# Optimization experiments

Hardware: AMD Instinct MI355X
Metric: run time of the kernel (lower is better)

## Reference

```python
import jax, jax.numpy as jnp
import numpy as np

B, IN_SIZE, OUT_SIZE, N_QUBITS, DEPTH = 4096, 512, 256, 12, 3
C64 = jnp.complex64
BN_EPS = 1e-5


def setup_inputs() -> dict:
    key = jax.random.key(0)
    ks = jax.random.split(key, 6)
    x = jax.random.normal(ks[0], (B, IN_SIZE), jnp.float32)
    enc_w = jax.random.normal(ks[1], (N_QUBITS, IN_SIZE), jnp.float32) / np.sqrt(IN_SIZE)
    enc_b = jnp.zeros((N_QUBITS,), jnp.float32)
    rot_params = jax.random.normal(ks[2], (DEPTH, N_QUBITS, 3), jnp.float32) * 0.1
    ent_params = jax.random.normal(ks[3], (DEPTH, N_QUBITS - 1), jnp.float32) * 0.1
    dec_w = jax.random.normal(ks[4], (OUT_SIZE, N_QUBITS), jnp.float32) / np.sqrt(N_QUBITS)
    dec_b = jnp.zeros((OUT_SIZE,), jnp.float32)
    return {
        'x': x, 'enc_w': enc_w, 'enc_b': enc_b,
        'rot_params': rot_params, 'ent_params': ent_params,
        'dec_w': dec_w, 'dec_b': dec_b,
        'bn1_gamma': jnp.ones((N_QUBITS,), jnp.float32),
        'bn1_beta': jnp.zeros((N_QUBITS,), jnp.float32),
        'bn2_gamma': jnp.ones((OUT_SIZE,), jnp.float32),
        'bn2_beta': jnp.zeros((OUT_SIZE,), jnp.float32),
    }


def _m2(a, b, c, d):
    return jnp.stack([jnp.stack([a, b]), jnp.stack([c, d])]).astype(C64)


def _rx(t):
    c = jnp.cos(t / 2).astype(C64)
    s = jnp.sin(t / 2).astype(C64)
    return _m2(c, -1j * s, -1j * s, c)


def _ry(t):
    c = jnp.cos(t / 2)
    s = jnp.sin(t / 2)
    return _m2(c, -s, s, c)


def _rz(p):
    z = jnp.zeros((), C64)
    return _m2(jnp.exp(-1j * p / 2), z, z, jnp.exp(1j * p / 2))


def _apply_1q(state, U, q):
    # state: [B, 2^n]; apply 2x2 U on qubit q (qubit 0 = most significant axis)
    b = state.shape[0]
    s = state.reshape(b, 2 ** q, 2, -1)
    s = jnp.einsum('ij,bkjl->bkil', U, s)
    return s.reshape(b, -1)


def _apply_cry(state, theta, q):
    # controlled-Ry: control qubit q, target qubit q+1 (adjacent)
    b = state.shape[0]
    R = _ry(theta)
    st = state.reshape(b, 2 ** q, 2, 2, -1)
    s0 = st[:, :, 0]
    s1 = jnp.einsum('ij,bkjl->bkil', R, st[:, :, 1])
    return jnp.stack([s0, s1], axis=2).reshape(b, -1)


def _batchnorm(x, g, b):
    # BatchNorm1d in training mode: biased batch stats
    m = x.mean(0)
    v = x.var(0)
    return g * (x - m) / jnp.sqrt(v + BN_EPS) + b


def _quantum_forward(encoded, rot_params, ent_params):
    # Batched statevector simulation of the per-sample circuit.
    b, n = encoded.shape
    depth = rot_params.shape[0]
    # amplitude encoding: normalize, theta = 2*arcsin(clip(|a|,0,1)), P(pi) if a<0
    norm = jnp.linalg.norm(encoded, axis=1, keepdims=True)
    a = jnp.where(norm > 0, encoded / jnp.maximum(norm, 1e-30), encoded)
    amp = jnp.clip(jnp.abs(a), 0.0, 1.0)              # sin(theta/2)
    cos_h = jnp.sqrt(jnp.maximum(1.0 - amp * amp, 0.0))  # cos(theta/2)
    sgn = jnp.where(a < 0, -1.0, 1.0)                  # P(pi) flips sign of |1> amp
    qvec = jnp.stack([cos_h, sgn * amp], axis=-1).astype(C64)  # [B, n, 2]
    # product state via successive outer products (loop over fixed n qubits)
    state = jnp.ones((b, 1), C64)
    for q in range(n):
        state = (state[:, :, None] * qvec[:, q, None, :]).reshape(b, -1)
    # parameterized circuit
    for l in range(depth):
        for q in range(n):
            U = _rz(rot_params[l, q, 2]) @ _ry(rot_params[l, q, 1]) @ _rx(rot_params[l, q, 0])
            state = _apply_1q(state, U, q)
        for q in range(n - 1):
            state = _apply_cry(state, ent_params[l, q], q)
    # per-qubit P(|1>) measurement probabilities
    idx = jnp.arange(2 ** n)
    bits = ((idx[:, None] >> (n - 1 - jnp.arange(n))) & 1).astype(jnp.float32)  # [2^n, n]
    probs = (jnp.abs(state) ** 2).astype(jnp.float32) @ bits  # [B, n]
    return probs


def reference(x, enc_w, enc_b, rot_params, ent_params, dec_w, dec_b,
              bn1_gamma, bn1_beta, bn2_gamma, bn2_beta):
    encoded = x @ enc_w.T + enc_b
    encoded = jnp.tanh(_batchnorm(encoded, bn1_gamma, bn1_beta))
    probs = _quantum_forward(encoded, rot_params, ent_params)
    out = probs @ dec_w.T + dec_b
    return _batchnorm(out, bn2_gamma, bn2_beta)
```

## Files before the change

### kernel.cpp

```cpp
#include <hip/hip_runtime.h>

#define BATCH   4096
#define IN_SZ   512
#define NQ      12
#define OUT_SZ  256
#define DEPTH   3
#define NST     4096
#define BN_EPS  1e-5f

#define OFF_ENC    0
#define OFF_BN1M   49152
#define OFF_BN1R   49168
#define OFF_GU     49184
#define OFF_GC     49472
#define OFF_GF     49568
#define OFF_PROBS  49792
#define OFF_PMEAN  98944
#define OFF_COV    98960
#define OFF_RSTD   99104

typedef float v2f __attribute__((ext_vector_type(2)));
typedef float v4f __attribute__((ext_vector_type(4)));
#define SW2(a) __builtin_shufflevector(a, a, 1, 0)

__global__ void k_encode(const float* __restrict__ x, const float* __restrict__ w,
                         const float* __restrict__ bvec,
                         const float* __restrict__ rot, const float* __restrict__ ent,
                         float* __restrict__ enc, float* __restrict__ gU, float* __restrict__ gC,
                         float* __restrict__ gF) {
    if (blockIdx.x == 1024) {
        int t = threadIdx.x;
        if (t < DEPTH * NQ) {
            float ax = rot[t * 3 + 0] * 0.5f;
            float ay = rot[t * 3 + 1] * 0.5f;
            float az = rot[t * 3 + 2] * 0.5f;
            float cx = cosf(ax), sx = sinf(ax);
            float cy = cosf(ay), sy = sinf(ay);
            float cz = cosf(az), sz = sinf(az);
            float m00r =  cy * cx, m00i =  sy * sx;
            float m01r = -sy * cx, m01i = -cy * sx;
            float m10r =  sy * cx, m10i = -cy * sx;
            float m11r =  cy * cx, m11i = -sy * sx;
            float* o = gU + t * 8;
            o[0] = cz * m00r + sz * m00i;  o[1] = cz * m00i - sz * m00r;
            o[2] = cz * m01r + sz * m01i;  o[3] = cz * m01i - sz * m01r;
            o[4] = cz * m10r - sz * m10i;  o[5] = cz * m10i + sz * m10r;
            o[6] = cz * m11r - sz * m11i;  o[7] = cz * m11i + sz * m11r;
        }
        if (t >= 64 && t - 64 < DEPTH * (NQ - 1)) {
            int i = t - 64;
            float th = ent[i] * 0.5f;
            gC[i * 2 + 0] = cosf(th);
            gC[i * 2 + 1] = sinf(th);
        }
        if (t >= 128 && t - 128 < DEPTH * 9) {
            int i = t - 128;
            int l = i / 9, k = i % 9;
            int c = k + k / 3;
            int tq = c + 1;
            const float* rr = rot + (l * NQ + tq) * 3;
            float ax = rr[0] * 0.5f, ay = rr[1] * 0.5f, az = rr[2] * 0.5f;
            float cx = cosf(ax), sx = sinf(ax);
            float cy = cosf(ay), sy = sinf(ay);
            float cz = cosf(az), sz = sinf(az);
            float m00r =  cy * cx, m00i =  sy * sx;
            float m01r = -sy * cx, m01i = -cy * sx;
            float m10r =  sy * cx, m10i = -cy * sx;
            float m11r =  cy * cx, m11i = -sy * sx;
            float u0 = cz * m00r + sz * m00i, u1 = cz * m00i - sz * m00r;
            float u2 = cz * m01r + sz * m01i, u3 = cz * m01i - sz * m01r;
            float u4 = cz * m10r - sz * m10i, u5 = cz * m10i + sz * m10r;
            float u6 = cz * m11r - sz * m11i, u7 = cz * m11i + sz * m11r;
            float th = ent[l * (NQ - 1) + c] * 0.5f;
            float c_ = cosf(th), s_ = sinf(th);
            float* o = gF + i * 8;
            o[0] = c_ * u0 - s_ * u4;  o[1] = c_ * u1 - s_ * u5;
            o[2] = c_ * u2 - s_ * u6;  o[3] = c_ * u3 - s_ * u7;
            o[4] = s_ * u0 + c_ * u4;  o[5] = s_ * u1 + c_ * u5;
            o[6] = s_ * u2 + c_ * u6;  o[7] = s_ * u3 + c_ * u7;
        }
        return;
    }
    int t = threadIdx.x;
    int wv = t >> 6, lane = t & 63;
    int row = blockIdx.x * 4 + wv;
    const float4* xr = (const float4*)(x + row * IN_SZ) + lane * 2;
    float4 xa = xr[0], xb = xr[1];
    float acc[NQ];
    #pragma unroll
    for (int q = 0; q < NQ; q++) {
        const float4* wr = (const float4*)(w + q * IN_SZ) + lane * 2;
        float4 wa = wr[0], wb = wr[1];
        float d = xa.x*wa.x + xa.y*wa.y + xa.z*wa.z + xa.w*wa.w
                + xb.x*wb.x + xb.y*wb.y + xb.z*wb.z + xb.w*wb.w;
        #pragma unroll
        for (int o = 32; o > 0; o >>= 1) d += __shfl_down(d, o, 64);
        acc[q] = d;
    }
    if (lane == 0) {
        float* er = enc + row * NQ;
        #pragma unroll
        for (int q = 0; q < NQ; q++) er[q] = acc[q] + bvec[q];
    }
}

__device__ float blockAllSum(float v, float* scr) {
    #pragma unroll
    for (int o = 32; o > 0; o >>= 1) v += __shfl_down(v, o, 64);
    int lane = threadIdx.x & 63, w = threadIdx.x >> 6;
    __syncthreads();
    if (lane == 0) scr[w] = v;
    __syncthreads();
    return scr[0] + scr[1] + scr[2] + scr[3];
}

__global__ void k_bnstats(const float* __restrict__ xm, float* __restrict__ mo,
                          float* __restrict__ ro) {
    __shared__ float scr[32];
    int j = blockIdx.x, t = threadIdx.x;
    float s = 0.f, s2 = 0.f;
    for (int b = t; b < BATCH; b += 1024) {
        float v = xm[b * NQ + j];
        s += v; s2 += v * v;
    }
    #pragma unroll
    for (int o = 32; o > 0; o >>= 1) { s += __shfl_down(s, o, 64); s2 += __shfl_down(s2, o, 64); }
    int lane = t & 63, w = t >> 6;
    if (lane == 0) { scr[w] = s; scr[16 + w] = s2; }
    __syncthreads();
    if (t == 0) {
        float S = 0.f, S2 = 0.f;
        #pragma unroll
        for (int i = 0; i < 16; i++) { S += scr[i]; S2 += scr[16 + i]; }
        float mean = S / (float)BATCH;
        float var  = S2 / (float)BATCH - mean * mean;
        mo[j] = mean;
        ro[j] = 1.f / sqrtf(var + BN_EPS);
    }
}

#define SLA2(j) ((T << 4) | ((((j) ^ ((T >> 1) & 7))) << 1))
#define SLB(m)  (((T & 0xF0) << 4) | ((m) << 4) | ((T & 15) ^ ((m) & 14)))
#define SLC(m)  (((m) << 8) | (T ^ ((((T >> 5) & 7)) << 1)))

#define LDA(j, Ra, Rb) { v4f t_ = *(const v4f*)(xch + SLA2(j));                 \
    Ra = __builtin_shufflevector(t_, t_, 0, 1);                                 \
    Rb = __builtin_shufflevector(t_, t_, 2, 3); }
#define STA(j, Ra, Rb) { v4f t_ = __builtin_shufflevector(Ra, Rb, 0, 1, 2, 3);  \
    *(v4f*)(xch + SLA2(j)) = t_; }

#define LOADA do { LDA(0,s0,s1) LDA(1,s2,s3) LDA(2,s4,s5) LDA(3,s6,s7)          \
    LDA(4,s8,s9) LDA(5,s10,s11) LDA(6,s12,s13) LDA(7,s14,s15) } while (0)
#define STORA do { STA(0,s0,s1) STA(1,s2,s3) STA(2,s4,s5) STA(3,s6,s7)          \
    STA(4,s8,s9) STA(5,s10,s11) STA(6,s12,s13) STA(7,s14,s15) } while (0)

#define LOADW(SL) do {                                                          \
    s0=xch[SL(0)];  s1=xch[SL(1)];  s2=xch[SL(2)];  s3=xch[SL(3)];              \
    s4=xch[SL(4)];  s5=xch[SL(5)];  s6=xch[SL(6)];  s7=xch[SL(7)];              \
    s8=xch[SL(8)];  s9=xch[SL(9)];  s10=xch[SL(10)]; s11=xch[SL(11)];           \
    s12=xch[SL(12)]; s13=xch[SL(13)]; s14=xch[SL(14)]; s15=xch[SL(15)]; } while (0)
#define STORW(SL) do {                                                          \
    xch[SL(0)]=s0;  xch[SL(1)]=s1;  xch[SL(2)]=s2;  xch[SL(3)]=s3;              \
    xch[SL(4)]=s4;  xch[SL(5)]=s5;  xch[SL(6)]=s6;  xch[SL(7)]=s7;              \
    xch[SL(8)]=s8;  xch[SL(9)]=s9;  xch[SL(10)]=s10; xch[SL(11)]=s11;           \
    xch[SL(12)]=s12; xch[SL(13)]=s13; xch[SL(14)]=s14; xch[SL(15)]=s15; } while (0)

#define U_LOADP(uptr) const float* u_ = (uptr);                                  \
    v2f c00r = {u_[0], u_[0]}, c00i = {-u_[1], u_[1]};                           \
    v2f c01r = {u_[2], u_[2]}, c01i = {-u_[3], u_[3]};                           \
    v2f c10r = {u_[4], u_[4]}, c10i = {-u_[5], u_[5]};                           \
    v2f c11r = {u_[6], u_[6]}, c11i = {-u_[7], u_[7]};

#define U_LOADF(uptr) const float* f_ = (uptr);                                  \
    v2f d00r = {f_[0], f_[0]}, d00i = {-f_[1], f_[1]};                           \
    v2f d01r = {f_[2], f_[2]}, d01i = {-f_[3], f_[3]};                           \
    v2f d10r = {f_[4], f_[4]}, d10i = {-f_[5], f_[5]};                           \
    v2f d11r = {f_[6], f_[6]}, d11i = {-f_[7], f_[7]};

#define U_PAIRP(A, B) { v2f a0 = A, a1 = B, a0s = SW2(a0), a1s = SW2(a1);        \
    A = a0*c00r + a0s*c00i + a1*c01r + a1s*c01i;                                 \
    B = a0*c10r + a0s*c10i + a1*c11r + a1s*c11i; }

#define U_PAIRF(A, B) { v2f a0 = A, a1 = B, a0s = SW2(a0), a1s = SW2(a1);        \
    A = a0*d00r + a0s*d00i + a1*d01r + a1s*d01i;                                 \
    B = a0*d10r + a0s*d10i + a1*d11r + a1s*d11i; }

#define APPLY_U_K3(uptr) do { U_LOADP(uptr)                                      \
    U_PAIRP(s0,s8) U_PAIRP(s1,s9) U_PAIRP(s2,s10) U_PAIRP(s3,s11)                \
    U_PAIRP(s4,s12) U_PAIRP(s5,s13) U_PAIRP(s6,s14) U_PAIRP(s7,s15) } while (0)

#define APPLY_UF_K2(uP, uF) do { U_LOADP(uP) U_LOADF(uF)                         \
    U_PAIRP(s0,s4) U_PAIRP(s1,s5) U_PAIRP(s2,s6) U_PAIRP(s3,s7)                  \
    U_PAIRF(s8,s12) U_PAIRF(s9,s13) U_PAIRF(s10,s14) U_PAIRF(s11,s15) } while (0)
#define APPLY_UF_K1(uP, uF) do { U_LOADP(uP) U_LOADF(uF)                         \
    U_PAIRP(s0,s2) U_PAIRP(s1,s3) U_PAIRF(s4,s6) U_PAIRF(s5,s7)                  \
    U_PAIRP(s8,s10) U_PAIRP(s9,s11) U_PAIRF(s12,s14) U_PAIRF(s13,s15) } while (0)
#define APPLY_UF_K0(uP, uF) do { U_LOADP(uP) U_LOADF(uF)                         \
    U_PAIRP(s0,s1) U_PAIRF(s2,s3) U_PAIRP(s4,s5) U_PAIRF(s6,s7)                  \
    U_PAIRP(s8,s9) U_PAIRF(s10,s11) U_PAIRP(s12,s13) U_PAIRF(s14,s15) } while (0)

#define RY_PAIRP(A, B) { v2f a0 = A, a1 = B;                                     \
    A = a0*cc2 - a1*ss2;  B = a0*ss2 + a1*cc2; }

#define RYALL_K3(cc, ss) do { v2f cc2 = {(cc),(cc)}, ss2 = {(ss),(ss)};          \
    RY_PAIRP(s0,s8) RY_PAIRP(s1,s9) RY_PAIRP(s2,s10) RY_PAIRP(s3,s11)            \
    RY_PAIRP(s4,s12) RY_PAIRP(s5,s13) RY_PAIRP(s6,s14) RY_PAIRP(s7,s15) } while (0)

#define INITJC(SR, j) { SR.x = f * (((j)&8)?qs0:qc0) * (((j)&4)?qs1:qc1)         \
    * (((j)&2)?qs2:qc2) * (((j)&1)?qs3:qc3); SR.y = 0.f; }
#define PRJ(S) ((S).x*(S).x + (S).y*(S).y)
#define WREDUCE(v) { v += __shfl_down(v,32,64); v += __shfl_down(v,16,64);       \
    v += __shfl_down(v,8,64); v += __shfl_down(v,4,64);                          \
    v += __shfl_down(v,2,64); v += __shfl_down(v,1,64); }

#define MKQ(i) float qc##i, qs##i; {                                             \
    float h_ = h##i;                                                             \
    float a_ = nz ? h_ * rinv : h_;                                              \
    float amp_ = fminf(fabsf(a_), 1.f);                                          \
    qc##i = sqrtf(fmaxf(1.f - amp_ * amp_, 0.f));                                \
    qs##i = (a_ < 0.f) ? -amp_ : amp_; }

__launch_bounds__(256)
__global__ void k_quantum(const float* __restrict__ enc,
                          const float* __restrict__ bn1m, const float* __restrict__ bn1r,
                          const float* __restrict__ g1, const float* __restrict__ b1,
                          const float* __restrict__ gU, const float* __restrict__ gC,
                          const float* __restrict__ gF,
                          float* __restrict__ probs) {
    __shared__ __align__(16) v2f xch[NST];

    int T = threadIdx.x, b = blockIdx.x;

    const float* er = enc + b * NQ;
    float h0  = tanhf(g1[0]  * (er[0]  - bn1m[0])  * bn1r[0]  + b1[0]);
    float h1  = tanhf(g1[1]  * (er[1]  - bn1m[1])  * bn1r[1]  + b1[1]);
    float h2  = tanhf(g1[2]  * (er[2]  - bn1m[2])  * bn1r[2]  + b1[2]);
    float h3  = tanhf(g1[3]  * (er[3]  - bn1m[3])  * bn1r[3]  + b1[3]);
    float h4  = tanhf(g1[4]  * (er[4]  - bn1m[4])  * bn1r[4]  + b1[4]);
    float h5  = tanhf(g1[5]  * (er[5]  - bn1m[5])  * bn1r[5]  + b1[5]);
    float h6  = tanhf(g1[6]  * (er[6]  - bn1m[6])  * bn1r[6]  + b1[6]);
    float h7  = tanhf(g1[7]  * (er[7]  - bn1m[7])  * bn1r[7]  + b1[7]);
    float h8  = tanhf(g1[8]  * (er[8]  - bn1m[8])  * bn1r[8]  + b1[8]);
    float h9  = tanhf(g1[9]  * (er[9]  - bn1m[9])  * bn1r[9]  + b1[9]);
    float h10 = tanhf(g1[10] * (er[10] - bn1m[10]) * bn1r[10] + b1[10]);
    float h11 = tanhf(g1[11] * (er[11] - bn1m[11]) * bn1r[11] + b1[11]);
    float n2 = h0*h0+h1*h1+h2*h2+h3*h3+h4*h4+h5*h5+h6*h6+h7*h7
             + h8*h8+h9*h9+h10*h10+h11*h11;
    float norm = sqrtf(n2);
    bool  nz   = norm > 0.f;
    float rinv = 1.f / fmaxf(norm, 1e-30f);
    MKQ(0) MKQ(1) MKQ(2) MKQ(3) MKQ(4) MKQ(5) MKQ(6) MKQ(7)
    MKQ(8) MKQ(9) MKQ(10) MKQ(11)

    v2f s0, s1, s2, s3, s4, s5, s6, s7, s8, s9, s10, s11, s12, s13, s14, s15;

    {
        float f = ((T>>7)&1 ? qs4 : qc4) * ((T>>6)&1 ? qs5 : qc5)
                * ((T>>5)&1 ? qs6 : qc6) * ((T>>4)&1 ? qs7 : qc7)
                * ((T>>3)&1 ? qs8 : qc8) * ((T>>2)&1 ? qs9 : qc9)
                * ((T>>1)&1 ? qs10 : qc10) * ((T>>0)&1 ? qs11 : qc11);
        INITJC(s0,0)  INITJC(s1,1)  INITJC(s2,2)  INITJC(s3,3)
        INITJC(s4,4)  INITJC(s5,5)  INITJC(s6,6)  INITJC(s7,7)
        INITJC(s8,8)  INITJC(s9,9)  INITJC(s10,10) INITJC(s11,11)
        INITJC(s12,12) INITJC(s13,13) INITJC(s14,14) INITJC(s15,15)
        APPLY_U_K3(gU + 0 * 8);
        APPLY_UF_K2(gU + 1 * 8, gF + 0 * 8);
        APPLY_UF_K1(gU + 2 * 8, gF + 1 * 8);
        APPLY_UF_K0(gU + 3 * 8, gF + 2 * 8);
        STORW(SLC);
    }
    __syncthreads();

    #pragma unroll 1
    for (int l = 0; l < DEPTH; l++) {
        const float* UL = gU + l * 96;
        const float* CL = gC + l * 22;
        const float* FL = gF + l * 72;
        LOADW(SLB);
        APPLY_U_K3(UL + 4 * 8);
        if (T & 16) RYALL_K3(CL[6], CL[7]);
        APPLY_UF_K2(UL + 5 * 8, FL + 3 * 8);
        APPLY_UF_K1(UL + 6 * 8, FL + 4 * 8);
        APPLY_UF_K0(UL + 7 * 8, FL + 5 * 8);
        STORW(SLB);
        __builtin_amdgcn_wave_barrier();
        LOADA;
        APPLY_U_K3(UL + 8 * 8);
        if (T & 1) RYALL_K3(CL[14], CL[15]);
        APPLY_UF_K2(UL + 9 * 8, FL + 6 * 8);
        APPLY_UF_K1(UL + 10 * 8, FL + 7 * 8);
        APPLY_UF_K0(UL + 11 * 8, FL + 8 * 8);
        if (l < DEPTH - 1) {
            STORA;
            __syncthreads();
            const float* UN = gU + (l + 1) * 96;
            const float* FN = gF + (l + 1) * 72;
            LOADW(SLC);
            APPLY_U_K3(UN + 0 * 8);
            APPLY_UF_K2(UN + 1 * 8, FN + 0 * 8);
            APPLY_UF_K1(UN + 2 * 8, FN + 1 * 8);
            APPLY_UF_K0(UN + 3 * 8, FN + 2 * 8);
            STORW(SLC);
            __syncthreads();
        }
    }

    float p0 = PRJ(s0),  p1 = PRJ(s1),  p2 = PRJ(s2),  p3 = PRJ(s3);
    float p4 = PRJ(s4),  p5 = PRJ(s5),  p6 = PRJ(s6),  p7 = PRJ(s7);
    float p8 = PRJ(s8),  p9 = PRJ(s9),  p10 = PRJ(s10), p11 = PRJ(s11);
    float p12 = PRJ(s12), p13 = PRJ(s13), p14 = PRJ(s14), p15 = PRJ(s15);
    float tot = p0+p1+p2+p3+p4+p5+p6+p7+p8+p9+p10+p11+p12+p13+p14+p15;
    float r8  = p8+p9+p10+p11+p12+p13+p14+p15;
    float r9  = p4+p5+p6+p7+p12+p13+p14+p15;
    float r10 = p2+p3+p6+p7+p10+p11+p14+p15;
    float r11 = p1+p3+p5+p7+p9+p11+p13+p15;
    float r0 = (T & 128) ? tot : 0.f;
    float r1 = (T & 64)  ? tot : 0.f;
    float r2 = (T & 32)  ? tot : 0.f;
    float r3 = (T & 16)  ? tot : 0.f;
    float r4 = (T & 8)   ? tot : 0.f;
    float r5 = (T & 4)   ? tot : 0.f;
    float r6 = (T & 2)   ? tot : 0.f;
    float r7 = (T & 1)   ? tot : 0.f;

    WREDUCE(r0) WREDUCE(r1) WREDUCE(r2) WREDUCE(r3) WREDUCE(r4) WREDUCE(r5)
    WREDUCE(r6) WREDUCE(r7) WREDUCE(r8) WREDUCE(r9) WREDUCE(r10) WREDUCE(r11)

    __syncthreads();
    float* red = (float*)xch;
    int lane = T & 63, w = T >> 6;
    if (lane == 0) {
        float* rr = red + w * NQ;
        rr[0]=r0; rr[1]=r1; rr[2]=r2; rr[3]=r3; rr[4]=r4; rr[5]=r5;
        rr[6]=r6; rr[7]=r7; rr[8]=r8; rr[9]=r9; rr[10]=r10; rr[11]=r11;
    }
    __syncthreads();
    if (T < NQ) probs[b * NQ + T] = red[T] + red[NQ + T] + red[2 * NQ + T] + red[3 * NQ + T];
}

__global__ void k_pcov(const float* __restrict__ probs, float* __restrict__ pmean,
                       float* __restrict__ cov) {
    __shared__ float scr[8];
    int blk = blockIdx.x;
    int q = blk / NQ, q2 = blk % NQ;
    int t = threadIdx.x;
    float sx = 0.f, sy = 0.f, sxy = 0.f;
    for (int b = t; b < BATCH; b += 256) {
        float xv = probs[b * NQ + q];
        float yv = probs[b * NQ + q2];
        sx += xv; sy += yv; sxy += xv * yv;
    }
    float SX  = blockAllSum(sx,  scr);
    float SY  = blockAllSum(sy,  scr);
    float SXY = blockAllSum(sxy, scr);
    if (t == 0) {
        float mx = SX / (float)BATCH, my = SY / (float)BATCH;
        cov[blk] = SXY / (float)BATCH - mx * my;
        if (q == q2) pmean[q] = mx;
    }
}

__global__ void k_rstd(const float* __restrict__ cov, const float* __restrict__ dw,
                       float* __restrict__ rstd) {
    __shared__ float cv[NQ * NQ];
    int t = threadIdx.x;
    if (t < NQ * NQ) cv[t] = cov[t];
    __syncthreads();
    float w[NQ];
    #pragma unroll
    for (int q = 0; q < NQ; q++) w[q] = dw[t * NQ + q];
    float var = 0.f;
    #pragma unroll
    for (int q = 0; q < NQ; q++) {
        float a = 0.f;
        #pragma unroll
        for (int q2 = 0; q2 < NQ; q2++) a += cv[q * NQ + q2] * w[q2];
        var += w[q] * a;
    }
    rstd[t] = 1.f / sqrtf(var + BN_EPS);
}

__global__ void k_final(const float* __restrict__ probs, const float* __restrict__ pmean,
                        const float* __restrict__ rstd, const float* __restrict__ dw,
                        const float* __restrict__ g2, const float* __restrict__ b2,
                        float* __restrict__ out) {
    __shared__ float cp[2][NQ];
    int b0 = blockIdx.x * 2;
    int t = threadIdx.x;
    int half = t >> 8, j = t & 255;
    if (t < NQ)                      cp[0][t]       = probs[b0 * NQ + t]        - pmean[t];
    else if (t >= 256 && t < 256+NQ) cp[1][t - 256] = probs[(b0+1) * NQ + t-256] - pmean[t - 256];
    __syncthreads();
    float acc = 0.f;
    #pragma unroll
    for (int q = 0; q < NQ; q++) acc += cp[half][q] * dw[j * NQ + q];
    out[(b0 + half) * OUT_SZ + j] = acc * rstd[j] * g2[j] + b2[j];
}

extern "C" void kernel_launch(void* const* d_in, const int* in_sizes, int n_in,
                              void* d_out, int out_size, void* d_ws, size_t ws_size,
                              hipStream_t stream) {
    const float* x     = (const float*)d_in[0];
    const float* enc_w = (const float*)d_in[1];
    const float* enc_b = (const float*)d_in[2];
    const float* rot   = (const float*)d_in[3];
    const float* ent   = (const float*)d_in[4];
    const float* dec_w = (const float*)d_in[5];
    const float* g1    = (const float*)d_in[7];
    const float* b1    = (const float*)d_in[8];
    const float* g2    = (const float*)d_in[9];
    const float* b2    = (const float*)d_in[10];

    float* ws    = (float*)d_ws;
    float* enc   = ws + OFF_ENC;
    float* bn1m  = ws + OFF_BN1M;
    float* bn1r  = ws + OFF_BN1R;
    float* gU    = ws + OFF_GU;
    float* gC    = ws + OFF_GC;
    float* gF    = ws + OFF_GF;
    float* prb   = ws + OFF_PROBS;
    float* pmean = ws + OFF_PMEAN;
    float* cov   = ws + OFF_COV;
    float* rstd  = ws + OFF_RSTD;

    hipLaunchKernelGGL(k_encode, dim3(1025), dim3(256), 0, stream,
                       x, enc_w, enc_b, rot, ent, enc, gU, gC, gF);
    hipLaunchKernelGGL(k_bnstats, dim3(NQ), dim3(1024), 0, stream, enc, bn1m, bn1r);
    hipLaunchKernelGGL(k_quantum, dim3(BATCH), dim3(256), 0, stream,
                       enc, bn1m, bn1r, g1, b1, gU, gC, gF, prb);
    hipLaunchKernelGGL(k_pcov, dim3(NQ * NQ), dim3(256), 0, stream, prb, pmean, cov);
    hipLaunchKernelGGL(k_rstd, dim3(1), dim3(OUT_SZ), 0, stream, cov, dec_w, rstd);
    hipLaunchKernelGGL(k_final, dim3(BATCH / 2), dim3(512), 0, stream,
                       prb, pmean, rstd, dec_w, g2, b2, (float*)d_out);
}
```

Baseline: 205.8 us.

## Fuse rstd into final kernel, parallelize qubit prep, factor state init and reductions

Removes the single-block k_rstd launch by having every k_final block recompute the per-output variance from the 12x12 covariance in shared memory, and reuses the loaded decoder weights. In k_quantum the per-sample tanh and normalization are computed by 16 lanes with shuffle reductions and broadcast through shared memory, instead of every thread doing 12 tanh calls. The initial state amplitudes are built with a shared product tree, and two wave reductions are replaced by deriving the top bits from the wave index. This trades one launch and redundant per-thread transcendentals for extra barriers and redundant covariance math in each final block.

```diff
diff --git a/kernel.cpp b/kernel.cpp
--- a/kernel.cpp
+++ b/kernel.cpp
@@ -17,7 +17,6 @@
 #define OFF_PROBS  49792
 #define OFF_PMEAN  98944
 #define OFF_COV    98960
-#define OFF_RSTD   99104
 
 typedef float v2f __attribute__((ext_vector_type(2)));
 typedef float v4f __attribute__((ext_vector_type(4)));
@@ -206,19 +205,10 @@
     RY_PAIRP(s0,s8) RY_PAIRP(s1,s9) RY_PAIRP(s2,s10) RY_PAIRP(s3,s11)            \
     RY_PAIRP(s4,s12) RY_PAIRP(s5,s13) RY_PAIRP(s6,s14) RY_PAIRP(s7,s15) } while (0)
 
-#define INITJC(SR, j) { SR.x = f * (((j)&8)?qs0:qc0) * (((j)&4)?qs1:qc1)         \
-    * (((j)&2)?qs2:qc2) * (((j)&1)?qs3:qc3); SR.y = 0.f; }
 #define PRJ(S) ((S).x*(S).x + (S).y*(S).y)
 #define WREDUCE(v) { v += __shfl_down(v,32,64); v += __shfl_down(v,16,64);       \
     v += __shfl_down(v,8,64); v += __shfl_down(v,4,64);                          \
     v += __shfl_down(v,2,64); v += __shfl_down(v,1,64); }
-
-#define MKQ(i) float qc##i, qs##i; {                                             \
-    float h_ = h##i;                                                             \
-    float a_ = nz ? h_ * rinv : h_;                                              \
-    float amp_ = fminf(fabsf(a_), 1.f);                                          \
-    qc##i = sqrtf(fmaxf(1.f - amp_ * amp_, 0.f));                                \
-    qs##i = (a_ < 0.f) ? -amp_ : amp_; }
 
 __launch_bounds__(256)
 __global__ void k_quantum(const float* __restrict__ enc,
@@ -231,26 +221,34 @@
 
     int T = threadIdx.x, b = blockIdx.x;
 
-    const float* er = enc + b * NQ;
-    float h0  = tanhf(g1[0]  * (er[0]  - bn1m[0])  * bn1r[0]  + b1[0]);
-    float h1  = tanhf(g1[1]  * (er[1]  - bn1m[1])  * bn1r[1]  + b1[1]);
-    float h2  = tanhf(g1[2]  * (er[2]  - bn1m[2])  * bn1r[2]  + b1[2]);
-    float h3  = tanhf(g1[3]  * (er[3]  - bn1m[3])  * bn1r[3]  + b1[3]);
-    float h4  = tanhf(g1[4]  * (er[4]  - bn1m[4])  * bn1r[4]  + b1[4]);
-    float h5  = tanhf(g1[5]  * (er[5]  - bn1m[5])  * bn1r[5]  + b1[5]);
-    float h6  = tanhf(g1[6]  * (er[6]  - bn1m[6])  * bn1r[6]  + b1[6]);
-    float h7  = tanhf(g1[7]  * (er[7]  - bn1m[7])  * bn1r[7]  + b1[7]);
-    float h8  = tanhf(g1[8]  * (er[8]  - bn1m[8])  * bn1r[8]  + b1[8]);
-    float h9  = tanhf(g1[9]  * (er[9]  - bn1m[9])  * bn1r[9]  + b1[9]);
-    float h10 = tanhf(g1[10] * (er[10] - bn1m[10]) * bn1r[10] + b1[10]);
-    float h11 = tanhf(g1[11] * (er[11] - bn1m[11]) * bn1r[11] + b1[11]);
-    float n2 = h0*h0+h1*h1+h2*h2+h3*h3+h4*h4+h5*h5+h6*h6+h7*h7
-             + h8*h8+h9*h9+h10*h10+h11*h11;
-    float norm = sqrtf(n2);
-    bool  nz   = norm > 0.f;
-    float rinv = 1.f / fmaxf(norm, 1e-30f);
-    MKQ(0) MKQ(1) MKQ(2) MKQ(3) MKQ(4) MKQ(5) MKQ(6) MKQ(7)
-    MKQ(8) MKQ(9) MKQ(10) MKQ(11)
+    float* qv = (float*)xch;
+    if (T < 16) {
+        float h = 0.f;
+        if (T < NQ) {
+            h = tanhf(g1[T] * (enc[b * NQ + T] - bn1m[T]) * bn1r[T] + b1[T]);
+        }
+        float n2 = h * h;
+        n2 += __shfl_xor(n2, 1, 16);
+        n2 += __shfl_xor(n2, 2, 16);
+        n2 += __shfl_xor(n2, 4, 16);
+        n2 += __shfl_xor(n2, 8, 16);
+        float norm = sqrtf(n2);
+        bool  nz   = norm > 0.f;
+        float rinv = 1.f / fmaxf(norm, 1e-30f);
+        float a_   = nz ? h * rinv : h;
+        float amp_ = fminf(fabsf(a_), 1.f);
+        float qc   = sqrtf(fmaxf(1.f - amp_ * amp_, 0.f));
+        float qs   = (a_ < 0.f) ? -amp_ : amp_;
+        if (T < NQ) { qv[T * 2] = qc; qv[T * 2 + 1] = qs; }
+    }
+    __syncthreads();
+    float qc0 = qv[0],  qs0 = qv[1],  qc1 = qv[2],  qs1 = qv[3];
+    float qc2 = qv[4],  qs2 = qv[5],  qc3 = qv[6],  qs3 = qv[7];
+    float qc4 = qv[8],  qs4 = qv[9],  qc5 = qv[10], qs5 = qv[11];
+    float qc6 = qv[12], qs6 = qv[13], qc7 = qv[14], qs7 = qv[15];
+    float qc8 = qv[16], qs8 = qv[17], qc9 = qv[18], qs9 = qv[19];
+    float qc10 = qv[20], qs10 = qv[21], qc11 = qv[22], qs11 = qv[23];
+    __syncthreads();
 
     v2f s0, s1, s2, s3, s4, s5, s6, s7, s8, s9, s10, s11, s12, s13, s14, s15;
 
@@ -259,10 +257,18 @@
                 * ((T>>5)&1 ? qs6 : qc6) * ((T>>4)&1 ? qs7 : qc7)
                 * ((T>>3)&1 ? qs8 : qc8) * ((T>>2)&1 ? qs9 : qc9)
                 * ((T>>1)&1 ? qs10 : qc10) * ((T>>0)&1 ? qs11 : qc11);
-        INITJC(s0,0)  INITJC(s1,1)  INITJC(s2,2)  INITJC(s3,3)
-        INITJC(s4,4)  INITJC(s5,5)  INITJC(s6,6)  INITJC(s7,7)
-        INITJC(s8,8)  INITJC(s9,9)  INITJC(s10,10) INITJC(s11,11)
-        INITJC(s12,12) INITJC(s13,13) INITJC(s14,14) INITJC(s15,15)
+        float p0c = f * qc0,  p0s = f * qs0;
+        float p00 = p0c*qc1, p01 = p0c*qs1, p10 = p0s*qc1, p11 = p0s*qs1;
+        float q000 = p00*qc2, q001 = p00*qs2, q010 = p01*qc2, q011 = p01*qs2;
+        float q100 = p10*qc2, q101 = p10*qs2, q110 = p11*qc2, q111 = p11*qs2;
+        s0  = (v2f){q000*qc3, 0.f};  s1  = (v2f){q000*qs3, 0.f};
+        s2  = (v2f){q001*qc3, 0.f};  s3  = (v2f){q001*qs3, 0.f};
+        s4  = (v2f){q010*qc3, 0.f};  s5  = (v2f){q010*qs3, 0.f};
+        s6  = (v2f){q011*qc3, 0.f};  s7  = (v2f){q011*qs3, 0.f};
+        s8  = (v2f){q100*qc3, 0.f};  s9  = (v2f){q100*qs3, 0.f};
+        s10 = (v2f){q101*qc3, 0.f};  s11 = (v2f){q101*qs3, 0.f};
+        s12 = (v2f){q110*qc3, 0.f};  s13 = (v2f){q110*qs3, 0.f};
+        s14 = (v2f){q111*qc3, 0.f};  s15 = (v2f){q111*qs3, 0.f};
         APPLY_U_K3(gU + 0 * 8);
         APPLY_UF_K2(gU + 1 * 8, gF + 0 * 8);
         APPLY_UF_K1(gU + 2 * 8, gF + 1 * 8);
@@ -314,8 +320,6 @@
     float r9  = p4+p5+p6+p7+p12+p13+p14+p15;
     float r10 = p2+p3+p6+p7+p10+p11+p14+p15;
     float r11 = p1+p3+p5+p7+p9+p11+p13+p15;
-    float r0 = (T & 128) ? tot : 0.f;
-    float r1 = (T & 64)  ? tot : 0.f;
     float r2 = (T & 32)  ? tot : 0.f;
     float r3 = (T & 16)  ? tot : 0.f;
     float r4 = (T & 8)   ? tot : 0.f;
@@ -323,15 +327,18 @@
     float r6 = (T & 2)   ? tot : 0.f;
     float r7 = (T & 1)   ? tot : 0.f;
 
-    WREDUCE(r0) WREDUCE(r1) WREDUCE(r2) WREDUCE(r3) WREDUCE(r4) WREDUCE(r5)
-    WREDUCE(r6) WREDUCE(r7) WREDUCE(r8) WREDUCE(r9) WREDUCE(r10) WREDUCE(r11)
+    WREDUCE(tot)
+    WREDUCE(r2) WREDUCE(r3) WREDUCE(r4) WREDUCE(r5) WREDUCE(r6) WREDUCE(r7)
+    WREDUCE(r8) WREDUCE(r9) WREDUCE(r10) WREDUCE(r11)
 
     __syncthreads();
     float* red = (float*)xch;
     int lane = T & 63, w = T >> 6;
     if (lane == 0) {
         float* rr = red + w * NQ;
-        rr[0]=r0; rr[1]=r1; rr[2]=r2; rr[3]=r3; rr[4]=r4; rr[5]=r5;
+        rr[0] = (w & 2) ? tot : 0.f;
+        rr[1] = (w & 1) ? tot : 0.f;
+        rr[2]=r2; rr[3]=r3; rr[4]=r4; rr[5]=r5;
         rr[6]=r6; rr[7]=r7; rr[8]=r8; rr[9]=r9; rr[10]=r10; rr[11]=r11;
     }
     __syncthreads();
@@ -360,41 +367,35 @@
     }
 }
 
-__global__ void k_rstd(const float* __restrict__ cov, const float* __restrict__ dw,
-                       float* __restrict__ rstd) {
-    __shared__ float cv[NQ * NQ];
-    int t = threadIdx.x;
-    if (t < NQ * NQ) cv[t] = cov[t];
-    __syncthreads();
-    float w[NQ];
-    #pragma unroll
-    for (int q = 0; q < NQ; q++) w[q] = dw[t * NQ + q];
-    float var = 0.f;
-    #pragma unroll
-    for (int q = 0; q < NQ; q++) {
-        float a = 0.f;
-        #pragma unroll
-        for (int q2 = 0; q2 < NQ; q2++) a += cv[q * NQ + q2] * w[q2];
-        var += w[q] * a;
-    }
-    rstd[t] = 1.f / sqrtf(var + BN_EPS);
-}
-
 __global__ void k_final(const float* __restrict__ probs, const float* __restrict__ pmean,
-                        const float* __restrict__ rstd, const float* __restrict__ dw,
+                        const float* __restrict__ cov, const float* __restrict__ dw,
                         const float* __restrict__ g2, const float* __restrict__ b2,
                         float* __restrict__ out) {
     __shared__ float cp[2][NQ];
+    __shared__ float cv[NQ * NQ];
     int b0 = blockIdx.x * 2;
     int t = threadIdx.x;
     int half = t >> 8, j = t & 255;
     if (t < NQ)                      cp[0][t]       = probs[b0 * NQ + t]        - pmean[t];
     else if (t >= 256 && t < 256+NQ) cp[1][t - 256] = probs[(b0+1) * NQ + t-256] - pmean[t - 256];
-    __syncthreads();
+    if (t >= 32 && t < 32 + NQ * NQ) cv[t - 32] = cov[t - 32];
+    __syncthreads();
+    float wv[NQ];
+    #pragma unroll
+    for (int q = 0; q < NQ; q++) wv[q] = dw[j * NQ + q];
+    float var = 0.f;
+    #pragma unroll
+    for (int q = 0; q < NQ; q++) {
+        float a = 0.f;
+        #pragma unroll
+        for (int q2 = 0; q2 < NQ; q2++) a += cv[q * NQ + q2] * wv[q2];
+        var += wv[q] * a;
+    }
+    float rstd = 1.f / sqrtf(var + BN_EPS);
     float acc = 0.f;
     #pragma unroll
-    for (int q = 0; q < NQ; q++) acc += cp[half][q] * dw[j * NQ + q];
-    out[(b0 + half) * OUT_SZ + j] = acc * rstd[j] * g2[j] + b2[j];
+    for (int q = 0; q < NQ; q++) acc += cp[half][q] * wv[q];
+    out[(b0 + half) * OUT_SZ + j] = acc * rstd * g2[j] + b2[j];
 }
 
 extern "C" void kernel_launch(void* const* d_in, const int* in_sizes, int n_in,
@@ -421,7 +422,6 @@
     float* prb   = ws + OFF_PROBS;
     float* pmean = ws + OFF_PMEAN;
     float* cov   = ws + OFF_COV;
-    float* rstd  = ws + OFF_RSTD;
 
     hipLaunchKernelGGL(k_encode, dim3(1025), dim3(256), 0, stream,
                        x, enc_w, enc_b, rot, ent, enc, gU, gC, gF);
@@ -429,7 +429,6 @@
     hipLaunchKernelGGL(k_quantum, dim3(BATCH), dim3(256), 0, stream,
                        enc, bn1m, bn1r, g1, b1, gU, gC, gF, prb);
     hipLaunchKernelGGL(k_pcov, dim3(NQ * NQ), dim3(256), 0, stream, prb, pmean, cov);
-    hipLaunchKernelGGL(k_rstd, dim3(1), dim3(OUT_SZ), 0, stream, cov, dec_w, rstd);
     hipLaunchKernelGGL(k_final, dim3(BATCH / 2), dim3(512), 0, stream,
-                       prb, pmean, rstd, dec_w, g2, b2, (float*)d_out);
-}
+                       prb, pmean, cov, dec_w, g2, b2, (float*)d_out);
+}
```

After: 200.8 us. 1.03x faster.
